# Performance work log

Hardware: AMD Instinct MI355X
Metric: run time of the kernel (lower is better)

Reference implementation:

```python
import jax, jax.numpy as jnp
import numpy as np

N = 100000
IN_DIM = 256
HID = 128
E = 1600000


def setup_inputs() -> dict:
    key = jax.random.key(0)
    ks = jax.random.split(key, 6)
    x = jax.random.normal(ks[0], (N, IN_DIM), dtype=jnp.float32)
    edge_index = jax.random.randint(ks[1], (2, E), 0, N, dtype=jnp.int64)
    # GCNConv weight (hidden, in) and bias (hidden); decoder Linear (in, hidden) + bias
    s_in = 1.0 / np.sqrt(IN_DIM)
    s_h = 1.0 / np.sqrt(HID)
    W_enc = jax.random.uniform(ks[2], (HID, IN_DIM), jnp.float32, -s_in, s_in)
    b_enc = jnp.zeros((HID,), jnp.float32)
    W_dec = jax.random.uniform(ks[3], (IN_DIM, HID), jnp.float32, -s_h, s_h)
    b_dec = jax.random.uniform(ks[4], (IN_DIM,), jnp.float32, -s_h, s_h)
    return {"x": x, "edge_index": edge_index, "W_enc": W_enc, "b_enc": b_enc,
            "W_dec": W_dec, "b_dec": b_dec}


def gcn_conv(x, edge_index, W, b):
    # Linear transform first (PyG GCNConv): h = x @ W^T  -> [N, HID]
    h = x @ W.T
    # Add self-loops
    loops = jnp.arange(N, dtype=edge_index.dtype)
    row = jnp.concatenate([edge_index[0], loops])  # source
    col = jnp.concatenate([edge_index[1], loops])  # target
    # Symmetric normalization: deg over targets (incl. self-loops)
    deg = jax.ops.segment_sum(jnp.ones_like(col, dtype=h.dtype), col, num_segments=N)
    dinv = jax.lax.rsqrt(deg)  # deg >= 1 due to self-loops
    norm = dinv[row] * dinv[col]  # [E+N]
    msg = h[row] * norm[:, None]  # gather + scale  [E+N, HID]
    agg = jax.ops.segment_sum(msg, col, num_segments=N)  # scatter-add
    return agg + b


def reference(x, edge_index, W_enc, b_enc, W_dec, b_dec):
    z = jax.nn.relu(gcn_conv(x, edge_index, W_enc, b_enc))
    x_recon = z @ W_dec.T + b_dec
    return (z, x_recon)
```

## Files before the change

kernel.cpp:

```cpp
#include <hip/hip_runtime.h>
#include <hip/hip_bf16.h>

#define NDIM 256
#define HDIM 128
#define NPAD 100352
#define LDS1_STRIDE 264
#define LDS2_STRIDE 136
#define P2CAP 6144

typedef __bf16 bf16_t;
typedef bf16_t bf16x2 __attribute__((ext_vector_type(2)));
typedef bf16_t bf16x4 __attribute__((ext_vector_type(4)));
typedef bf16_t bf16x8 __attribute__((ext_vector_type(8)));
typedef float f32x4 __attribute__((ext_vector_type(4)));

__global__ __launch_bounds__(256) void k_prep(const float* __restrict__ We, bf16_t* __restrict__ wpe,
                                              const float* __restrict__ Wd, bf16_t* __restrict__ wpd) {
    const int b = blockIdx.x, t = threadIdx.x;
    const bool enc = b < 16;
    const int i = (enc ? b : b - 16) * 256 + t;
    const int lane = i & 63;
    const int fr = lane & 15, kg = lane >> 4;
    int nf, kk32, K, NF;
    const float* W;
    bf16_t* wp;
    if (enc) { nf = (i >> 6) & 7;  kk32 = i >> 9;  K = NDIM; NF = 8;  W = We; wp = wpe; }
    else     { nf = (i >> 6) & 15; kk32 = i >> 10; K = HDIM; NF = 16; W = Wd; wp = wpd; }
    const float* src = &W[(size_t)(nf * 16 + fr) * K + kk32 * 32 + kg * 8];
    const f32x4 a0 = *reinterpret_cast<const f32x4*>(src);
    const f32x4 a1 = *reinterpret_cast<const f32x4*>(src + 4);
    bf16x8 o;
    o[0] = (bf16_t)a0[0]; o[1] = (bf16_t)a0[1]; o[2] = (bf16_t)a0[2]; o[3] = (bf16_t)a0[3];
    o[4] = (bf16_t)a1[0]; o[5] = (bf16_t)a1[1]; o[6] = (bf16_t)a1[2]; o[7] = (bf16_t)a1[3];
    reinterpret_cast<bf16x8*>(wp)[(kk32 * NF + nf) * 64 + lane] = o;
}

template<int K, int NC, bool OUT_BF16>
__device__ __forceinline__ void mfma_epi(const bf16x8* af,
                                         const bf16_t* __restrict__ Wp,
                                         const float* __restrict__ bias,
                                         void* __restrict__ Cout,
                                         const int bid, const int nrows) {
    const int lane = threadIdx.x & 63;
    const int wv = threadIdx.x >> 6;
    const int fr = lane & 15;
    const int kg = lane >> 4;
    constexpr int NF = NC / 16, NK = K / 32;

    const bf16x8* wp = reinterpret_cast<const bf16x8*>(Wp);
    f32x4 acc[NF];
    const f32x4 zero4 = {0.f, 0.f, 0.f, 0.f};
    #pragma unroll
    for (int nf = 0; nf < NF; ++nf) acc[nf] = zero4;

    #pragma unroll
    for (int k = 0; k < NK; ++k) {
        #pragma unroll
        for (int nf = 0; nf < NF; ++nf)
            acc[nf] = __builtin_amdgcn_mfma_f32_16x16x32_bf16(af[k], wp[(k * NF + nf) * 64 + lane], acc[nf], 0, 0, 0);
    }

    const long long rbase = (long long)bid * 64 + wv * 16 + kg * 4;
    #pragma unroll
    for (int nf = 0; nf < NF; ++nf) {
        const int c = nf * 16 + fr;
        const float bv = bias ? bias[c] : 0.f;
        #pragma unroll
        for (int i = 0; i < 4; ++i) {
            const long long r = rbase + i;
            if (r < nrows) {
                const float v = acc[nf][i] + bv;
                if (OUT_BF16) ((bf16_t*)Cout)[r * NC + c] = (bf16_t)v;
                else          ((float*)Cout)[r * NC + c] = v;
            }
        }
    }
}

__device__ __forceinline__ void gemm1_body(const int bid, const float* __restrict__ x,
                                           const bf16_t* __restrict__ wpe,
                                           bf16_t* __restrict__ hb, const int nrows,
                                           bf16_t* lds) {
    const int t = threadIdx.x;
    const long long rowbase = (long long)bid * 64;
    #pragma unroll
    for (int p = 0; p < 16; ++p) {
        const int s = p * 256 + t;
        const int r = s >> 6, c4 = s & 63;
        long long gr = rowbase + r;
        if (gr >= nrows) gr = nrows - 1;
        const f32x4 v = *reinterpret_cast<const f32x4*>(&x[gr * NDIM + c4 * 4]);
        bf16x4 o;
        o[0] = (bf16_t)v[0]; o[1] = (bf16_t)v[1]; o[2] = (bf16_t)v[2]; o[3] = (bf16_t)v[3];
        *reinterpret_cast<bf16x4*>(&lds[r * LDS1_STRIDE + c4 * 4]) = o;
    }
    __syncthreads();
    const int lane = t & 63, wv = t >> 6, fr = lane & 15, kg = lane >> 4;
    bf16x8 af[8];
    #pragma unroll
    for (int k = 0; k < 8; ++k)
        af[k] = *reinterpret_cast<const bf16x8*>(&lds[(wv * 16 + fr) * LDS1_STRIDE + k * 32 + kg * 8]);
    mfma_epi<NDIM, HDIM, true>(af, wpe, nullptr, hb, bid, nrows);
}

__device__ __forceinline__ void p1a_body(const int blk, const int* __restrict__ col,
                                         int* __restrict__ bcnt, const int E_,
                                         const int nbkt, const int epb, int* lhist) {
    const int t = threadIdx.x;
    for (int i = t; i < nbkt; i += 256) lhist[i] = 0;
    __syncthreads();
    const int base = blk * epb;
    const int cnt = min(E_ - base, epb);
    for (int i = t; i < cnt; i += 256)
        atomicAdd(&lhist[col[base + i] >> 8], 1);
    __syncthreads();
    for (int i = t; i < nbkt; i += 256)
        bcnt[i * 256 + blk] = lhist[i];
}

__global__ __launch_bounds__(256) void k_fused(const float* __restrict__ x,
                                               const bf16_t* __restrict__ wpe,
                                               bf16_t* __restrict__ hb, const int nrows,
                                               const int* __restrict__ col,
                                               int* __restrict__ bcnt,
                                               const int E_, const int nbkt, const int epb,
                                               const int G1) {
    __shared__ __align__(16) bf16_t lds[64 * LDS1_STRIDE];
    const int b = blockIdx.x;
    if (b < G1) gemm1_body(b, x, wpe, hb, nrows, lds);
    else        p1a_body(b - G1, col, bcnt, E_, nbkt, epb, (int*)lds);
}

__global__ __launch_bounds__(256) void k_scanB1(const int* __restrict__ bcnt,
                                                int* __restrict__ bsum, const int M) {
    __shared__ int s[256];
    const int b = blockIdx.x, t = threadIdx.x;
    const int i0 = b * 1024 + t * 4;
    int4 v = make_int4(0, 0, 0, 0);
    if (i0 + 4 <= M) v = *reinterpret_cast<const int4*>(&bcnt[i0]);
    else if (i0 < M) {
        const int k = M - i0;
        v.x = bcnt[i0];
        if (k > 1) v.y = bcnt[i0 + 1];
        if (k > 2) v.z = bcnt[i0 + 2];
    }
    s[t] = v.x + v.y + v.z + v.w;
    __syncthreads();
    for (int d = 128; d > 0; d >>= 1) {
        if (t < d) s[t] += s[t + d];
        __syncthreads();
    }
    if (t == 0) bsum[b] = s[0];
}

__global__ __launch_bounds__(128) void k_scanB2(const int* __restrict__ bsum,
                                                int* __restrict__ bofs,
                                                int* __restrict__ bbase,
                                                const int nb, const int M) {
    __shared__ int s[128];
    const int t = threadIdx.x;
    const int v = (t < nb) ? bsum[t] : 0;
    s[t] = v;
    __syncthreads();
    for (int d = 1; d < 128; d <<= 1) {
        int xx = (t >= d) ? s[t - d] : 0;
        __syncthreads();
        s[t] += xx;
        __syncthreads();
    }
    if (t < nb) bofs[t] = s[t] - v;
    if (t == nb - 1) bbase[M] = s[t];
}

__global__ __launch_bounds__(256) void k_scanB3(const int* __restrict__ bcnt,
                                                const int* __restrict__ bofs,
                                                int* __restrict__ bbase, const int M) {
    __shared__ int s[256];
    const int b = blockIdx.x, t = threadIdx.x;
    const int i0 = b * 1024 + t * 4;
    int4 v = make_int4(0, 0, 0, 0);
    if (i0 + 4 <= M) v = *reinterpret_cast<const int4*>(&bcnt[i0]);
    else if (i0 < M) {
        const int k = M - i0;
        v.x = bcnt[i0];
        if (k > 1) v.y = bcnt[i0 + 1];
        if (k > 2) v.z = bcnt[i0 + 2];
    }
    const int tsum = v.x + v.y + v.z + v.w;
    s[t] = tsum;
    __syncthreads();
    for (int d = 1; d < 256; d <<= 1) {
        int xx = (t >= d) ? s[t - d] : 0;
        __syncthreads();
        s[t] += xx;
        __syncthreads();
    }
    const int excl = s[t] - tsum + bofs[b];
    int4 o;
    o.x = excl; o.y = excl + v.x; o.z = o.y + v.y; o.w = o.z + v.z;
    if (i0 + 4 <= M) *reinterpret_cast<int4*>(&bbase[i0]) = o;
    else if (i0 < M) {
        const int k = M - i0;
        bbase[i0] = o.x;
        if (k > 1) bbase[i0 + 1] = o.y;
        if (k > 2) bbase[i0 + 2] = o.z;
    }
}

__global__ __launch_bounds__(256) void k_p1b(const int* __restrict__ row,
                                             const int* __restrict__ col,
                                             const int* __restrict__ bbase,
                                             int2* __restrict__ pbuf,
                                             const int E_, const int nbkt, const int epb) {
    __shared__ int lcur[512];
    const int blk = blockIdx.x, t = threadIdx.x;
    for (int i = t; i < nbkt; i += 256) lcur[i] = bbase[i * 256 + blk];
    __syncthreads();
    const int base = blk * epb;
    const int cnt = min(E_ - base, epb);
    for (int i = t; i < cnt; i += 256) {
        const int c = col[base + i];
        const int r = row[base + i];
        const int pos = atomicAdd(&lcur[c >> 8], 1);
        pbuf[pos] = make_int2(r, c);
    }
}

__global__ __launch_bounds__(256) void k_p2(const int2* __restrict__ pbuf,
                                            const int* __restrict__ bbase,
                                            int* __restrict__ ebuf,
                                            int* __restrict__ goff, int* __restrict__ gcnt,
                                            float* __restrict__ dinv,
                                            const int n, const int E_) {
    __shared__ int lcnt[256], lscan[256], lcur[256];
    __shared__ __align__(16) int2 ecache[P2CAP];
    const int b = blockIdx.x, t = threadIdx.x;
    const int start = bbase[b * 256];
    const int end = bbase[(b + 1) * 256];
    const int size = end - start;
    const bool inlds = size <= P2CAP;
    lcnt[t] = 0; lcur[t] = 0;
    __syncthreads();
    if (inlds) {
        for (int i = t; i < size; i += 256) {
            const int2 e = pbuf[start + i];
            ecache[i] = e;
            atomicAdd(&lcnt[e.y & 255], 1);
        }
    } else {
        for (int i = t; i < size; i += 256)
            atomicAdd(&lcnt[pbuf[start + i].y & 255], 1);
    }
    __syncthreads();
    const int v = lcnt[t];
    lscan[t] = v;
    __syncthreads();
    for (int d = 1; d < 256; d <<= 1) {
        int xx = (t >= d) ? lscan[t - d] : 0;
        __syncthreads();
        lscan[t] += xx;
        __syncthreads();
    }
    const int excl = lscan[t] - v;
    const int node = (b << 8) + t;
    if (node < n) {
        goff[node] = start + excl;
        gcnt[node] = v;
        dinv[node] = rsqrtf((float)(v + 1));
    }
    lscan[t] = excl;
    __syncthreads();
    for (int i = t; i < size; i += 256) {
        const int2 e = inlds ? ecache[i] : pbuf[start + i];
        const int li = e.y & 255;
        const int rk = atomicAdd(&lcur[li], 1);
        ebuf[start + lscan[li] + rk] = e.x;
    }
}

__device__ __forceinline__ float bflo(unsigned u) { return __uint_as_float(u << 16); }
__device__ __forceinline__ float bfhi(unsigned u) { return __uint_as_float(u & 0xffff0000u); }

__global__ __launch_bounds__(256) void k_agg(const int* __restrict__ ebuf,
                                             const int* __restrict__ off,
                                             const int* __restrict__ cnt,
                                             const float* __restrict__ dinv,
                                             const unsigned* __restrict__ hb,
                                             const float* __restrict__ benc,
                                             float* __restrict__ z,
                                             bf16_t* __restrict__ zb, int n) {
    const int node = blockIdx.x * 4 + (threadIdx.x >> 6);
    const int lane = threadIdx.x & 63;
    if (node >= n) return;
    const float dc = dinv[node];
    const unsigned hself = hb[(size_t)node * 64 + lane];
    float acc0 = bflo(hself) * (dc * dc);
    float acc1 = bfhi(hself) * (dc * dc);
    const int base = off[node], m = cnt[node];
    int j = 0;
    for (; j + 16 <= m; j += 16) {
        int r[16]; float d[16]; unsigned u[16];
        #pragma unroll
        for (int q = 0; q < 16; ++q) r[q] = ebuf[base + j + q];
        #pragma unroll
        for (int q = 0; q < 16; ++q) u[q] = hb[(size_t)r[q] * 64 + lane];
        #pragma unroll
        for (int q = 0; q < 16; ++q) d[q] = dinv[r[q]];
        #pragma unroll
        for (int q = 0; q < 16; ++q) {
            const float nq = d[q] * dc;
            acc0 += bflo(u[q]) * nq;
            acc1 += bfhi(u[q]) * nq;
        }
    }
    for (; j + 4 <= m; j += 4) {
        int r[4]; float d[4]; unsigned u[4];
        #pragma unroll
        for (int q = 0; q < 4; ++q) r[q] = ebuf[base + j + q];
        #pragma unroll
        for (int q = 0; q < 4; ++q) u[q] = hb[(size_t)r[q] * 64 + lane];
        #pragma unroll
        for (int q = 0; q < 4; ++q) d[q] = dinv[r[q]];
        #pragma unroll
        for (int q = 0; q < 4; ++q) {
            const float nq = d[q] * dc;
            acc0 += bflo(u[q]) * nq;
            acc1 += bfhi(u[q]) * nq;
        }
    }
    for (; j < m; ++j) {
        const int r = ebuf[base + j];
        const float nr = dinv[r] * dc;
        const unsigned u = hb[(size_t)r * 64 + lane];
        acc0 += bflo(u) * nr;
        acc1 += bfhi(u) * nr;
    }
    float2 o;
    o.x = fmaxf(acc0 + benc[lane * 2], 0.f);
    o.y = fmaxf(acc1 + benc[lane * 2 + 1], 0.f);
    *reinterpret_cast<float2*>(&z[(size_t)node * HDIM + lane * 2]) = o;
    bf16x2 ob;
    ob[0] = (bf16_t)o.x;
    ob[1] = (bf16_t)o.y;
    *reinterpret_cast<bf16x2*>(&zb[(size_t)node * HDIM + lane * 2]) = ob;
}

__global__ __launch_bounds__(256) void k_gemm2(const bf16_t* __restrict__ zb,
                                               const bf16_t* __restrict__ wpd,
                                               const float* __restrict__ bias,
                                               float* __restrict__ xrec, const int nrows) {
    __shared__ __align__(16) bf16_t lds[64 * LDS2_STRIDE];
    const int t = threadIdx.x;
    const long long rowbase = (long long)blockIdx.x * 64;
    #pragma unroll
    for (int p = 0; p < 4; ++p) {
        const int s = p * 256 + t;
        const int r = s >> 4, c8 = s & 15;
        long long gr = rowbase + r;
        if (gr >= nrows) gr = nrows - 1;
        const bf16x8 v = *reinterpret_cast<const bf16x8*>(&zb[gr * HDIM + c8 * 8]);
        *reinterpret_cast<bf16x8*>(&lds[r * LDS2_STRIDE + c8 * 8]) = v;
    }
    __syncthreads();
    const int lane = t & 63, wv = t >> 6, fr = lane & 15, kg = lane >> 4;
    bf16x8 af[4];
    #pragma unroll
    for (int k = 0; k < 4; ++k)
        af[k] = *reinterpret_cast<const bf16x8*>(&lds[(wv * 16 + fr) * LDS2_STRIDE + k * 32 + kg * 8]);
    mfma_epi<HDIM, NDIM, false>(af, wpd, bias, xrec, blockIdx.x, nrows);
}

extern "C" void kernel_launch(void* const* d_in, const int* in_sizes, int n_in,
                              void* d_out, int out_size, void* d_ws, size_t ws_size,
                              hipStream_t stream) {
    const float* x     = (const float*)d_in[0];
    const int*   ei    = (const int*)d_in[1];
    const float* W_enc = (const float*)d_in[2];
    const float* b_enc = (const float*)d_in[3];
    const float* W_dec = (const float*)d_in[4];
    const float* b_dec = (const float*)d_in[5];

    const int N = in_sizes[0] / NDIM;
    const int E = in_sizes[1] / 2;
    const int* row = ei;
    const int* col = ei + E;

    const int NBKT = (N + 255) >> 8;
    const int M = NBKT * 256;
    const int EPB = (E + 255) / 256;
    const int G1 = (N + 63) / 64;
    const int SB = (M + 1023) / 1024;

    char* wsp = (char*)d_ws;
    int2*   pbuf = (int2*)wsp;
    bf16_t* zb   = (bf16_t*)wsp;
    const size_t r0 = ((size_t)N * HDIM * 2 > (size_t)E * 8) ? (size_t)N * HDIM * 2 : (size_t)E * 8;
    bf16_t* hb   = (bf16_t*)(wsp + r0);
    int*    ebuf = (int*)(wsp + r0 + (size_t)N * HDIM * 2);
    int*    goff = ebuf + E;
    int*    gcnt = goff + NPAD;
    float*  dinv = (float*)(gcnt + NPAD);
    int*    bcnt = (int*)(dinv + NPAD);
    int*    bbase = bcnt + M;
    int*    bsum = bbase + M + 1;
    int*    bofs = bsum + 128;
    bf16_t* wpe  = (bf16_t*)(bofs + 128);
    bf16_t* wpd  = wpe + HDIM * NDIM;

    float* z    = (float*)d_out;
    float* xrec = (float*)d_out + (size_t)N * HDIM;

    k_prep<<<32, 256, 0, stream>>>(W_enc, wpe, W_dec, wpd);

    k_fused<<<G1 + 256, 256, 0, stream>>>(x, wpe, hb, N, col, bcnt, E, NBKT, EPB, G1);

    k_scanB1<<<SB, 256, 0, stream>>>(bcnt, bsum, M);
    k_scanB2<<<1, 128, 0, stream>>>(bsum, bofs, bbase, SB, M);
    k_scanB3<<<SB, 256, 0, stream>>>(bcnt, bofs, bbase, M);

    k_p1b<<<256, 256, 0, stream>>>(row, col, bbase, pbuf, E, NBKT, EPB);

    k_p2<<<NBKT, 256, 0, stream>>>(pbuf, bbase, ebuf, goff, gcnt, dinv, N, E);

    k_agg<<<(N + 3) / 4, 256, 0, stream>>>(ebuf, goff, gcnt, dinv, (const unsigned*)hb, b_enc, z, zb, N);

    k_gemm2<<<G1, 256, 0, stream>>>(zb, wpd, b_dec, xrec, N);
}
```

Baseline: 246.1 us.

## Pack edge pairs into one int and split wave across two neighbors in aggregation

Edge bucketing now stores each (row, col-low-byte) pair as a single 32-bit word instead of an int2, halving pbuf traffic and LDS cache size in the partition kernels. The aggregation kernel splits each 64-lane wave into two half-waves that each read 8-byte chunks of a different neighbor's bf16 row, then combines them with a shuffle. This is meant to increase gather width per lane and memory-level parallelism. The packing assumes node ids fit in 17 bits, which holds for N=100000 but would break for larger graphs.

```diff
diff --git a/kernel.cpp b/kernel.cpp
--- a/kernel.cpp
+++ b/kernel.cpp
@@ -210,7 +210,7 @@
 __global__ __launch_bounds__(256) void k_p1b(const int* __restrict__ row,
                                              const int* __restrict__ col,
                                              const int* __restrict__ bbase,
-                                             int2* __restrict__ pbuf,
+                                             int* __restrict__ pbuf,
                                              const int E_, const int nbkt, const int epb) {
     __shared__ int lcur[512];
     const int blk = blockIdx.x, t = threadIdx.x;
@@ -222,18 +222,18 @@
         const int c = col[base + i];
         const int r = row[base + i];
         const int pos = atomicAdd(&lcur[c >> 8], 1);
-        pbuf[pos] = make_int2(r, c);
-    }
-}
-
-__global__ __launch_bounds__(256) void k_p2(const int2* __restrict__ pbuf,
+        pbuf[pos] = r | ((c & 255) << 17);
+    }
+}
+
+__global__ __launch_bounds__(256) void k_p2(const int* __restrict__ pbuf,
                                             const int* __restrict__ bbase,
                                             int* __restrict__ ebuf,
                                             int* __restrict__ goff, int* __restrict__ gcnt,
                                             float* __restrict__ dinv,
                                             const int n, const int E_) {
     __shared__ int lcnt[256], lscan[256], lcur[256];
-    __shared__ __align__(16) int2 ecache[P2CAP];
+    __shared__ __align__(16) int ecache[P2CAP];
     const int b = blockIdx.x, t = threadIdx.x;
     const int start = bbase[b * 256];
     const int end = bbase[(b + 1) * 256];
@@ -243,13 +243,13 @@
     __syncthreads();
     if (inlds) {
         for (int i = t; i < size; i += 256) {
-            const int2 e = pbuf[start + i];
+            const int e = pbuf[start + i];
             ecache[i] = e;
-            atomicAdd(&lcnt[e.y & 255], 1);
+            atomicAdd(&lcnt[(e >> 17) & 255], 1);
         }
     } else {
         for (int i = t; i < size; i += 256)
-            atomicAdd(&lcnt[pbuf[start + i].y & 255], 1);
+            atomicAdd(&lcnt[(pbuf[start + i] >> 17) & 255], 1);
     }
     __syncthreads();
     const int v = lcnt[t];
@@ -271,10 +271,10 @@
     lscan[t] = excl;
     __syncthreads();
     for (int i = t; i < size; i += 256) {
-        const int2 e = inlds ? ecache[i] : pbuf[start + i];
-        const int li = e.y & 255;
+        const int e = inlds ? ecache[i] : pbuf[start + i];
+        const int li = (e >> 17) & 255;
         const int rk = atomicAdd(&lcur[li], 1);
-        ebuf[start + lscan[li] + rk] = e.x;
+        ebuf[start + lscan[li] + rk] = e & 0x1FFFF;
     }
 }
 
@@ -285,64 +285,71 @@
                                              const int* __restrict__ off,
                                              const int* __restrict__ cnt,
                                              const float* __restrict__ dinv,
-                                             const unsigned* __restrict__ hb,
+                                             const uint2* __restrict__ hb2,
                                              const float* __restrict__ benc,
                                              float* __restrict__ z,
                                              bf16_t* __restrict__ zb, int n) {
     const int node = blockIdx.x * 4 + (threadIdx.x >> 6);
     const int lane = threadIdx.x & 63;
+    const int l2 = lane & 31;
+    const int h = lane >> 5;
     if (node >= n) return;
     const float dc = dinv[node];
-    const unsigned hself = hb[(size_t)node * 64 + lane];
-    float acc0 = bflo(hself) * (dc * dc);
-    float acc1 = bfhi(hself) * (dc * dc);
+    float a0 = 0.f, a1 = 0.f, a2 = 0.f, a3 = 0.f;
+    if (h == 0) {
+        const uint2 us = hb2[(size_t)node * 32 + l2];
+        const float s = dc * dc;
+        a0 = bflo(us.x) * s; a1 = bfhi(us.x) * s;
+        a2 = bflo(us.y) * s; a3 = bfhi(us.y) * s;
+    }
     const int base = off[node], m = cnt[node];
     int j = 0;
     for (; j + 16 <= m; j += 16) {
-        int r[16]; float d[16]; unsigned u[16];
-        #pragma unroll
-        for (int q = 0; q < 16; ++q) r[q] = ebuf[base + j + q];
-        #pragma unroll
-        for (int q = 0; q < 16; ++q) u[q] = hb[(size_t)r[q] * 64 + lane];
-        #pragma unroll
-        for (int q = 0; q < 16; ++q) d[q] = dinv[r[q]];
-        #pragma unroll
-        for (int q = 0; q < 16; ++q) {
+        int r[8]; float d[8]; uint2 u[8];
+        #pragma unroll
+        for (int q = 0; q < 8; ++q) r[q] = ebuf[base + j + 2 * q + h];
+        #pragma unroll
+        for (int q = 0; q < 8; ++q) u[q] = hb2[(size_t)r[q] * 32 + l2];
+        #pragma unroll
+        for (int q = 0; q < 8; ++q) d[q] = dinv[r[q]];
+        #pragma unroll
+        for (int q = 0; q < 8; ++q) {
             const float nq = d[q] * dc;
-            acc0 += bflo(u[q]) * nq;
-            acc1 += bfhi(u[q]) * nq;
+            a0 += bflo(u[q].x) * nq; a1 += bfhi(u[q].x) * nq;
+            a2 += bflo(u[q].y) * nq; a3 += bfhi(u[q].y) * nq;
         }
     }
-    for (; j + 4 <= m; j += 4) {
-        int r[4]; float d[4]; unsigned u[4];
-        #pragma unroll
-        for (int q = 0; q < 4; ++q) r[q] = ebuf[base + j + q];
-        #pragma unroll
-        for (int q = 0; q < 4; ++q) u[q] = hb[(size_t)r[q] * 64 + lane];
-        #pragma unroll
-        for (int q = 0; q < 4; ++q) d[q] = dinv[r[q]];
-        #pragma unroll
-        for (int q = 0; q < 4; ++q) {
-            const float nq = d[q] * dc;
-            acc0 += bflo(u[q]) * nq;
-            acc1 += bfhi(u[q]) * nq;
-        }
-    }
-    for (; j < m; ++j) {
+    for (; j + 2 <= m; j += 2) {
+        const int r = ebuf[base + j + h];
+        const float nq = dinv[r] * dc;
+        const uint2 u = hb2[(size_t)r * 32 + l2];
+        a0 += bflo(u.x) * nq; a1 += bfhi(u.x) * nq;
+        a2 += bflo(u.y) * nq; a3 += bfhi(u.y) * nq;
+    }
+    if (j < m && h == 0) {
         const int r = ebuf[base + j];
-        const float nr = dinv[r] * dc;
-        const unsigned u = hb[(size_t)r * 64 + lane];
-        acc0 += bflo(u) * nr;
-        acc1 += bfhi(u) * nr;
-    }
-    float2 o;
-    o.x = fmaxf(acc0 + benc[lane * 2], 0.f);
-    o.y = fmaxf(acc1 + benc[lane * 2 + 1], 0.f);
-    *reinterpret_cast<float2*>(&z[(size_t)node * HDIM + lane * 2]) = o;
-    bf16x2 ob;
-    ob[0] = (bf16_t)o.x;
-    ob[1] = (bf16_t)o.y;
-    *reinterpret_cast<bf16x2*>(&zb[(size_t)node * HDIM + lane * 2]) = ob;
+        const float nq = dinv[r] * dc;
+        const uint2 u = hb2[(size_t)r * 32 + l2];
+        a0 += bflo(u.x) * nq; a1 += bfhi(u.x) * nq;
+        a2 += bflo(u.y) * nq; a3 += bfhi(u.y) * nq;
+    }
+    a0 += __shfl(a0, lane ^ 32);
+    a1 += __shfl(a1, lane ^ 32);
+    a2 += __shfl(a2, lane ^ 32);
+    a3 += __shfl(a3, lane ^ 32);
+    if (h == 0) {
+        const float4 bb = *reinterpret_cast<const float4*>(&benc[l2 * 4]);
+        float4 o;
+        o.x = fmaxf(a0 + bb.x, 0.f);
+        o.y = fmaxf(a1 + bb.y, 0.f);
+        o.z = fmaxf(a2 + bb.z, 0.f);
+        o.w = fmaxf(a3 + bb.w, 0.f);
+        *reinterpret_cast<float4*>(&z[(size_t)node * HDIM + l2 * 4]) = o;
+        bf16x4 ob;
+        ob[0] = (bf16_t)o.x; ob[1] = (bf16_t)o.y;
+        ob[2] = (bf16_t)o.z; ob[3] = (bf16_t)o.w;
+        *reinterpret_cast<bf16x4*>(&zb[(size_t)node * HDIM + l2 * 4]) = ob;
+    }
 }
 
 __global__ __launch_bounds__(256) void k_gemm2(const bf16_t* __restrict__ zb,
@@ -392,9 +399,9 @@
     const int SB = (M + 1023) / 1024;
 
     char* wsp = (char*)d_ws;
-    int2*   pbuf = (int2*)wsp;
+    int*    pbuf = (int*)wsp;
     bf16_t* zb   = (bf16_t*)wsp;
-    const size_t r0 = ((size_t)N * HDIM * 2 > (size_t)E * 8) ? (size_t)N * HDIM * 2 : (size_t)E * 8;
+    const size_t r0 = ((size_t)N * HDIM * 2 > (size_t)E * 4) ? (size_t)N * HDIM * 2 : (size_t)E * 4;
     bf16_t* hb   = (bf16_t*)(wsp + r0);
     int*    ebuf = (int*)(wsp + r0 + (size_t)N * HDIM * 2);
     int*    goff = ebuf + E;
@@ -422,7 +429,7 @@
 
     k_p2<<<NBKT, 256, 0, stream>>>(pbuf, bbase, ebuf, goff, gcnt, dinv, N, E);
 
-    k_agg<<<(N + 3) / 4, 256, 0, stream>>>(ebuf, goff, gcnt, dinv, (const unsigned*)hb, b_enc, z, zb, N);
+    k_agg<<<(N + 3) / 4, 256, 0, stream>>>(ebuf, goff, gcnt, dinv, (const uint2*)hb, b_enc, z, zb, N);
 
     k_gemm2<<<G1, 256, 0, stream>>>(zb, wpd, b_dec, xrec, N);
 }
```

After: 246.8 us. Within noise of the previous version (+0.3%).
